# Kernel tuning notes

Measured on AMD Instinct MI355X. Metric: run time of the kernel, lower is better.

## Reference

```python
import jax, jax.numpy as jnp
import numpy as np

N_EMBED = 1024
EMBED_DIM = 64
BETA = 0.25


def setup_inputs() -> dict:
    key = jax.random.key(0)
    k1, k2 = jax.random.split(key)
    # z_e: (B, C, H, W) with C == embed_dim
    z_e = jax.random.normal(k1, (16, EMBED_DIM, 64, 64), dtype=jnp.float32)
    # codebook init: uniform(-1/n_embed, 1/n_embed), matching nn.init.uniform_
    emb = jax.random.uniform(k2, (N_EMBED, EMBED_DIM), dtype=jnp.float32,
                             minval=-1.0 / N_EMBED, maxval=1.0 / N_EMBED)
    return {"z_e": z_e, "emb": emb}


def reference(z_e, emb):
    B, C, H, W = z_e.shape
    # (B,C,H,W) -> (B,H,W,C) -> (B*H*W, C)
    z_flat = jnp.transpose(z_e, (0, 2, 3, 1)).reshape(-1, C)
    # squared euclidean distances to every codebook entry: (N, n_embed)
    dist = (jnp.sum(z_flat * z_flat, axis=1, keepdims=True)
            - 2.0 * (z_flat @ emb.T)
            + jnp.sum(emb * emb, axis=1)[None, :])
    idx = jnp.argmin(dist, axis=1)  # (N,)
    # gather codebook vectors, back to (B, C, H, W)
    z_q = jnp.transpose(emb[idx].reshape(B, H, W, C), (0, 3, 1, 2))
    # straight-through estimator
    z_q_st = z_e + jax.lax.stop_gradient(z_q - z_e)
    codebook_loss = jnp.mean((jax.lax.stop_gradient(z_q) - z_e) ** 2)
    commit_loss = jnp.mean((z_q - jax.lax.stop_gradient(z_e)) ** 2)
    loss = codebook_loss + BETA * commit_loss
    return z_q_st, loss, idx.reshape(B, H, W)
```

## Files before the change

kernel.cpp:

```cpp
#include <hip/hip_runtime.h>

#define NROWS   65536
#define NEMB    1024
#define HWD     4096
#define CHW     262144
#define OUT_ZQ  4194304
#define BETA    0.25f
#define MARGIN  6e-3f
#define MAXC    32

typedef __attribute__((ext_vector_type(8))) short bf16x8;
typedef __attribute__((ext_vector_type(4))) float f32x4;

#define F4C(v,i) ((i)==0?(v).x:((i)==1?(v).y:((i)==2?(v).z:(v).w)))

__device__ __forceinline__ unsigned short bf16rn(float f) {
    unsigned int x = __float_as_uint(f);
    x += 0x7fffu + ((x >> 16) & 1);
    return (unsigned short)(x >> 16);
}
__device__ __forceinline__ float bf16tof(unsigned short h) {
    return __uint_as_float(((unsigned int)h) << 16);
}
__device__ __forceinline__ unsigned int ordf(float f) {
    unsigned int u = __float_as_uint(f);
    return (u & 0x80000000u) ? ~u : (u | 0x80000000u);
}
__device__ __forceinline__ float deordf(unsigned int m) {
    return __uint_as_float((m & 0x80000000u) ? (m ^ 0x80000000u) : ~m);
}

__device__ __forceinline__ float np_pairwise64(const float p[64]) {
#pragma clang fp contract(off)
    float r[8];
#pragma unroll
    for (int a = 0; a < 8; ++a) r[a] = p[a];
#pragma unroll
    for (int i = 8; i < 64; i += 8) {
#pragma unroll
        for (int a = 0; a < 8; ++a) r[a] = r[a] + p[i + a];
    }
    return ((r[0] + r[1]) + (r[2] + r[3])) + ((r[4] + r[5]) + (r[6] + r[7]));
}

__global__ void k_prep(const float* __restrict__ emb, bf16x8* __restrict__ ebt,
                       float* __restrict__ se) {
#pragma clang fp contract(off)
    int idx  = blockIdx.x * 256 + threadIdx.x;
    int tile = idx >> 7;
    int f    = (idx >> 6) & 1;
    int lane = idx & 63;
    int entry = tile * 16 + (lane & 15);
    int kb    = f * 32 + ((lane >> 4) << 3);
    bf16x8 v;
#pragma unroll
    for (int i = 0; i < 8; ++i)
        v[i] = (short)bf16rn(emb[(size_t)entry * 64 + kb + i]);
    ebt[idx] = v;

    if (blockIdx.x < 4) {
        int j = blockIdx.x * 256 + threadIdx.x;
        float p[64];
#pragma unroll
        for (int c = 0; c < 64; ++c) { float vv = emb[(size_t)j * 64 + c]; p[c] = vv * vv; }
        se[j] = np_pairwise64(p);
    }
}

__global__ __launch_bounds__(256, 2) void k_mfma(
        const float* __restrict__ ze, const float* __restrict__ emb,
        const bf16x8* __restrict__ ebt, const float* __restrict__ se,
        float* __restrict__ out, float* __restrict__ wsloss) {
#pragma clang fp contract(off)
    __shared__ float zt[4096];
    __shared__ unsigned short zb[4096];
    __shared__ float se_s[NEMB];
    __shared__ float sz_s[64];
    __shared__ unsigned int rowmin_u[64];
    __shared__ int cnt_s[64];
    __shared__ int cand_s[64 * MAXC];
    __shared__ unsigned long long best_s[64];
    __shared__ int bi_s[64];

    const int tid  = threadIdx.x;
    const int wid  = tid >> 6;
    const int lane = tid & 63;
    const int l15  = lane & 15;
    const int kg   = lane >> 4;
    const int row0 = blockIdx.x * 64;
    const int b    = row0 >> 12;
    const int hw0  = row0 & 4095;
    const float* __restrict__ zblk = ze + (size_t)b * CHW + hw0;

#pragma unroll
    for (int k = 0; k < 4; ++k) se_s[k * 256 + tid] = se[k * 256 + tid];
#pragma unroll
    for (int k = 0; k < 16; ++k) {
        int idx = k * 256 + tid;
        zt[idx] = zblk[(size_t)(idx >> 6) * HWD + (idx & 63)];
    }
    if (tid < 64) { rowmin_u[tid] = 0xFFFFFFFFu; cnt_s[tid] = 0; best_s[tid] = ~0ULL; }
    __syncthreads();

    if (tid < 64) {
        float p[64];
#pragma unroll
        for (int c = 0; c < 64; ++c) { float v = zt[c * 64 + tid]; p[c] = v * v; }
        sz_s[tid] = np_pairwise64(p);
    }

#pragma unroll
    for (int k4 = 0; k4 < 2; ++k4) {
        int cid = k4 * 256 + tid;
        int row = cid >> 3, kc = cid & 7;
        bf16x8 v;
#pragma unroll
        for (int i = 0; i < 8; ++i) {
            int k = kc * 8 + i;
            v[i] = (short)bf16rn(zt[k * 64 + row]);
        }
        *(bf16x8*)&zb[(row * 64 + kc * 8) ^ ((row & 7) << 3)] = v;
    }
    __syncthreads();

    const int arow  = wid * 16 + l15;
    const int abase = arow * 64 + kg * 8;
    const int aswz  = (arow & 7) << 3;
    const bf16x8 Ah0 = *(const bf16x8*)&zb[(abase +  0) ^ aswz];
    const bf16x8 Ah1 = *(const bf16x8*)&zb[(abase + 32) ^ aswz];

    float rmin[4] = {3.4028235e38f, 3.4028235e38f, 3.4028235e38f, 3.4028235e38f};
    const bf16x8* __restrict__ ebt_l = ebt + lane;
    const f32x4 zero4 = {0.0f, 0.0f, 0.0f, 0.0f};
    bf16x8 Ca, Cb, Na, Nb;

#define LOADB(T, Xa, Xb) do {                                               \
        const bf16x8* p_ = ebt_l + (T) * 128;                               \
        Xa = p_[0]; Xb = p_[64];                                            \
    } while (0)

#define PROCESS(T, Xa, Xb, PASS2) do {                                      \
        f32x4 acc_ = zero4;                                                 \
        acc_ = __builtin_amdgcn_mfma_f32_16x16x32_bf16(Ah0, Xa, acc_, 0,0,0);\
        acc_ = __builtin_amdgcn_mfma_f32_16x16x32_bf16(Ah1, Xb, acc_, 0,0,0);\
        const int j_ = (T) * 16 + l15;                                      \
        const float sej_ = se_s[j_];                                        \
        _Pragma("unroll")                                                   \
        for (int q = 0; q < 4; ++q) {                                       \
            float g_ = fmaf(-2.0f, F4C(acc_, q), sej_);                     \
            if (!(PASS2)) {                                                 \
                rmin[q] = fminf(rmin[q], g_);                               \
            } else if (g_ <= rmin[q]) {                                     \
                int row_ = wid * 16 + kg * 4 + q;                           \
                int k_ = atomicAdd(&cnt_s[row_], 1);                        \
                if (k_ < MAXC) cand_s[row_ * MAXC + k_] = j_;               \
            }                                                               \
        }                                                                   \
    } while (0)

    LOADB(0, Ca, Cb);
    for (int t = 0; t < 64; t += 2) {
        LOADB(t + 1, Na, Nb);
        PROCESS(t, Ca, Cb, false);
        LOADB((t + 2 > 63 ? 63 : t + 2), Ca, Cb);
        PROCESS(t + 1, Na, Nb, false);
    }
#pragma unroll
    for (int q = 0; q < 4; ++q)
        atomicMin(&rowmin_u[wid * 16 + kg * 4 + q], ordf(rmin[q]));
    __syncthreads();
#pragma unroll
    for (int q = 0; q < 4; ++q)
        rmin[q] = deordf(rowmin_u[wid * 16 + kg * 4 + q]) + MARGIN;

    LOADB(0, Ca, Cb);
    for (int t = 0; t < 64; t += 2) {
        LOADB(t + 1, Na, Nb);
        PROCESS(t, Ca, Cb, true);
        LOADB((t + 2 > 63 ? 63 : t + 2), Ca, Cb);
        PROCESS(t + 1, Na, Nb, true);
    }
    __syncthreads();

    for (int w = tid; w < 64 * MAXC; w += 256) {
        int r = w >> 5, ci = w & (MAXC - 1);
        int nc = cnt_s[r];
        if (ci < (nc < MAXC ? nc : MAXC)) {
            int j = cand_s[r * MAXC + ci];
            const float* __restrict__ e = emb + (size_t)j * 64;
            float dot = 0.0f;
#pragma unroll
            for (int c = 0; c < 64; ++c) dot = fmaf(e[c], zt[c * 64 + r], dot);
            float d = (sz_s[r] - 2.0f * dot) + se_s[j];
            atomicMin(&best_s[r],
                      ((unsigned long long)ordf(d) << 32) | (unsigned int)j);
        }
        if (nc > MAXC) {
            for (int j = ci; j < NEMB; j += MAXC) {
                const float* __restrict__ e = emb + (size_t)j * 64;
                float dot = 0.0f;
#pragma unroll
                for (int c = 0; c < 64; ++c) dot = fmaf(e[c], zt[c * 64 + r], dot);
                float d = (sz_s[r] - 2.0f * dot) + se_s[j];
                atomicMin(&best_s[r],
                          ((unsigned long long)ordf(d) << 32) | (unsigned int)j);
            }
        }
    }
    __syncthreads();

    if (tid < 64) {
        int j = (int)(best_s[tid] & 0xFFFFFFFFu);
        bi_s[tid] = j;
        out[(size_t)OUT_ZQ + 1 + row0 + tid] = (float)j;
    }
    __syncthreads();

    float part = 0.0f;
#pragma unroll
    for (int rep = 0; rep < 16; ++rep) {
        int i = rep * 256 + tid;
        int c = i >> 6, r = i & 63;
        int bj = bi_s[r];
        size_t zoff = (size_t)b * CHW + (size_t)c * HWD + hw0 + r;
        float ev = emb[(size_t)bj * 64 + c];
        float zv = ze[zoff];
        float qmz = ev - zv;
        out[zoff] = zv + qmz;
        part = part + qmz * qmz;
    }
    float* red_s = (float*)cand_s;
    red_s[tid] = part;
    __syncthreads();
#pragma unroll
    for (int s = 128; s >= 1; s >>= 1) {
        if (tid < s) red_s[tid] = red_s[tid] + red_s[tid + s];
        __syncthreads();
    }
    if (tid == 0) wsloss[blockIdx.x] = red_s[0];
#undef LOADB
#undef PROCESS
}

__global__ __launch_bounds__(256, 4) void k_main_v5(
        const float* __restrict__ ze, const float* __restrict__ emb,
        const float* __restrict__ se, float* __restrict__ out,
        float* __restrict__ wsloss) {
#pragma clang fp contract(off)
    __shared__ float zt[4096];
    __shared__ float es[4096];
    __shared__ float se_s[NEMB];
    __shared__ float sz_s[64];
    __shared__ int   bi_s[64];

    const int tid  = threadIdx.x;
    const int rg   = tid & 15;
    const int eg   = tid >> 4;
    const int row0 = blockIdx.x * 64;
    const int b    = row0 >> 12;
    const int hw0  = row0 & 4095;
    const float* __restrict__ zblk = ze + (size_t)b * CHW + hw0;

#pragma unroll
    for (int k = 0; k < 4; ++k) se_s[k * 256 + tid] = se[k * 256 + tid];
#pragma unroll
    for (int k = 0; k < 16; ++k) {
        int idx = k * 256 + tid;
        zt[idx] = zblk[(size_t)(idx >> 6) * HWD + (idx & 63)];
    }
    __syncthreads();
    if (tid < 64) {
        float p[64];
#pragma unroll
        for (int c = 0; c < 64; ++c) { float v = zt[c * 64 + tid]; p[c] = v * v; }
        sz_s[tid] = np_pairwise64(p);
    }
    __syncthreads();
    const float4 sz4 = *(const float4*)&sz_s[rg * 4];
    float best[4] = {3.4028235e38f, 3.4028235e38f, 3.4028235e38f, 3.4028235e38f};
    int   bi[4]   = {0, 0, 0, 0};
    for (int ch = 0; ch < 16; ++ch) {
        __syncthreads();
        {
            const float4* __restrict__ src = (const float4*)(emb + ch * 4096);
#pragma unroll
            for (int k = 0; k < 4; ++k) {
                int idx = k * 256 + tid;
                int jl = idx >> 4, c4 = idx & 15;
                *(float4*)&es[(jl << 6) + ((c4 ^ (jl & 15)) << 2)] = src[idx];
            }
        }
        __syncthreads();
        const float4 se4 = *(const float4*)&se_s[ch * 64 + eg * 4];
        float acc[4][4];
#pragma unroll
        for (int a = 0; a < 4; ++a)
#pragma unroll
            for (int q = 0; q < 4; ++q) acc[a][q] = 0.0f;
#pragma unroll 4
        for (int c4 = 0; c4 < 16; ++c4) {
            float4 zq[4], ef[4];
#pragma unroll
            for (int cc = 0; cc < 4; ++cc)
                zq[cc] = *(const float4*)&zt[((c4 * 4 + cc) << 6) + (rg << 2)];
#pragma unroll
            for (int jj = 0; jj < 4; ++jj) {
                int jl = eg * 4 + jj;
                ef[jj] = *(const float4*)&es[(jl << 6) + ((c4 ^ (jl & 15)) << 2)];
            }
#pragma unroll
            for (int cc = 0; cc < 4; ++cc)
#pragma unroll
                for (int jj = 0; jj < 4; ++jj)
#pragma unroll
                    for (int rr = 0; rr < 4; ++rr)
                        acc[jj][rr] = fmaf(F4C(ef[jj], cc), F4C(zq[cc], rr), acc[jj][rr]);
        }
        const int j0 = ch * 64 + eg * 4;
#pragma unroll
        for (int jj = 0; jj < 4; ++jj) {
            float sej = F4C(se4, jj);
#pragma unroll
            for (int rr = 0; rr < 4; ++rr) {
                float dist = (F4C(sz4, rr) - 2.0f * acc[jj][rr]) + sej;
                if (dist < best[rr]) { best[rr] = dist; bi[rr] = j0 + jj; }
            }
        }
    }
    __syncthreads();
    float* dmin_s = zt;
    int*   imin_s = (int*)es;
#pragma unroll
    for (int rr = 0; rr < 4; ++rr) {
        dmin_s[tid * 4 + rr] = best[rr];
        imin_s[tid * 4 + rr] = bi[rr];
    }
    __syncthreads();
    if (tid < 64) {
        int rgm = tid >> 2, rrm = tid & 3;
        float bb = 3.4028235e38f; int ii = 0x7fffffff;
#pragma unroll
        for (int m = 0; m < 16; ++m) {
            int t = m * 16 + rgm;
            float d  = dmin_s[t * 4 + rrm];
            int   i2 = imin_s[t * 4 + rrm];
            if (d < bb || (d == bb && i2 < ii)) { bb = d; ii = i2; }
        }
        bi_s[tid] = ii;
        out[(size_t)OUT_ZQ + 1 + row0 + tid] = (float)ii;
    }
    __syncthreads();
    float part = 0.0f;
#pragma unroll
    for (int rep = 0; rep < 16; ++rep) {
        int i = rep * 256 + tid;
        int c = i >> 6, r = i & 63;
        int bj = bi_s[r];
        size_t zoff = (size_t)b * CHW + (size_t)c * HWD + hw0 + r;
        float ev = emb[(size_t)bj * 64 + c];
        float zv = ze[zoff];
        float qmz = ev - zv;
        out[zoff] = zv + qmz;
        part = part + qmz * qmz;
    }
    float* red_s = zt;
    red_s[tid] = part;
    __syncthreads();
#pragma unroll
    for (int s = 128; s >= 1; s >>= 1) {
        if (tid < s) red_s[tid] = red_s[tid] + red_s[tid + s];
        __syncthreads();
    }
    if (tid == 0) wsloss[blockIdx.x] = red_s[0];
}

__global__ void k_loss(const float* __restrict__ wsloss, float* __restrict__ out) {
#pragma clang fp contract(off)
    __shared__ float red[256];
    int tid = threadIdx.x;
    float s = 0.0f;
    for (int i = tid; i < 1024; i += 256) s = s + wsloss[i];
    red[tid] = s;
    __syncthreads();
#pragma unroll
    for (int k = 128; k >= 1; k >>= 1) {
        if (tid < k) red[tid] = red[tid] + red[tid + k];
        __syncthreads();
    }
    if (tid == 0) {
        float mse = red[0] / 4194304.0f;
        out[OUT_ZQ] = mse + BETA * mse;
    }
}

extern "C" void kernel_launch(void* const* d_in, const int* in_sizes, int n_in,
                              void* d_out, int out_size, void* d_ws, size_t ws_size,
                              hipStream_t stream) {
    const float* ze  = (const float*)d_in[0];
    const float* emb = (const float*)d_in[1];
    float* out    = (float*)d_out;
    float* se     = (float*)d_ws;
    float* wsloss = se + NEMB;
    bf16x8* ebt   = (bf16x8*)(wsloss + 1024);
    const size_t NEED = 2048 * sizeof(float) + 8192 * sizeof(bf16x8);

    if (ws_size >= NEED) {
        k_prep<<<32,   256, 0, stream>>>(emb, ebt, se);
        k_mfma<<<1024, 256, 0, stream>>>(ze, emb, ebt, se, out, wsloss);
    } else {
        k_prep<<<32, 256, 0, stream>>>(emb, (bf16x8*)d_ws, se);
        k_main_v5<<<1024, 256, 0, stream>>>(ze, emb, se, out, wsloss);
    }
    k_loss<<<1, 256, 0, stream>>>(wsloss, out);
}
```

Measured before the change: 130.4 us.

## Use split-bf16 A operand in MFMA screening, halve rows per block

The z operand becomes a hi+lo bf16 pair, so each 16x16 tile now takes four MFMAs instead of two. This gives more accurate screening distances, which lets the margin shrink and the per-row candidate cap drop from 32 to 16. Each block now handles 32 rows, with the four waves split as two row halves by two codebook halves, and the grid doubles to 2048 blocks. The aim is fewer fp32 rescoring candidates, less LDS per block and more blocks in flight, at the cost of twice the MFMA work and a higher chance of the fallback path when more than 16 candidates survive.

Result: slower. 173.4 us (+33.0%).

```diff
diff --git a/kernel.cpp b/kernel.cpp
--- a/kernel.cpp
+++ b/kernel.cpp
@@ -6,8 +6,8 @@
 #define CHW     262144
 #define OUT_ZQ  4194304
 #define BETA    0.25f
-#define MARGIN  6e-3f
-#define MAXC    32
+#define MARGIN  4e-3f
+#define MAXC    16
 
 typedef __attribute__((ext_vector_type(8))) short bf16x8;
 typedef __attribute__((ext_vector_type(4))) float f32x4;
@@ -72,22 +72,24 @@
         const bf16x8* __restrict__ ebt, const float* __restrict__ se,
         float* __restrict__ out, float* __restrict__ wsloss) {
 #pragma clang fp contract(off)
-    __shared__ float zt[4096];
+    __shared__ float zt[2048];
     __shared__ unsigned short zb[4096];
     __shared__ float se_s[NEMB];
-    __shared__ float sz_s[64];
-    __shared__ unsigned int rowmin_u[64];
-    __shared__ int cnt_s[64];
-    __shared__ int cand_s[64 * MAXC];
-    __shared__ unsigned long long best_s[64];
-    __shared__ int bi_s[64];
+    __shared__ float sz_s[32];
+    __shared__ unsigned int rowmin_u[32];
+    __shared__ int cnt_s[32];
+    __shared__ int cand_s[32 * MAXC];
+    __shared__ unsigned long long best_s[32];
+    __shared__ int bi_s[32];
 
     const int tid  = threadIdx.x;
     const int wid  = tid >> 6;
     const int lane = tid & 63;
     const int l15  = lane & 15;
     const int kg   = lane >> 4;
-    const int row0 = blockIdx.x * 64;
+    const int rh   = wid >> 1;
+    const int eh   = wid & 1;
+    const int row0 = blockIdx.x * 32;
     const int b    = row0 >> 12;
     const int hw0  = row0 & 4095;
     const float* __restrict__ zblk = ze + (size_t)b * CHW + hw0;
@@ -95,42 +97,46 @@
 #pragma unroll
     for (int k = 0; k < 4; ++k) se_s[k * 256 + tid] = se[k * 256 + tid];
 #pragma unroll
-    for (int k = 0; k < 16; ++k) {
+    for (int k = 0; k < 8; ++k) {
         int idx = k * 256 + tid;
-        zt[idx] = zblk[(size_t)(idx >> 6) * HWD + (idx & 63)];
-    }
-    if (tid < 64) { rowmin_u[tid] = 0xFFFFFFFFu; cnt_s[tid] = 0; best_s[tid] = ~0ULL; }
-    __syncthreads();
-
-    if (tid < 64) {
+        zt[idx] = zblk[(size_t)(idx >> 5) * HWD + (idx & 31)];
+    }
+    if (tid < 32) { rowmin_u[tid] = 0xFFFFFFFFu; cnt_s[tid] = 0; best_s[tid] = ~0ULL; }
+    __syncthreads();
+
+    if (tid < 32) {
         float p[64];
 #pragma unroll
-        for (int c = 0; c < 64; ++c) { float v = zt[c * 64 + tid]; p[c] = v * v; }
+        for (int c = 0; c < 64; ++c) { float v = zt[c * 32 + tid]; p[c] = v * v; }
         sz_s[tid] = np_pairwise64(p);
     }
 
 #pragma unroll
     for (int k4 = 0; k4 < 2; ++k4) {
         int cid = k4 * 256 + tid;
-        int row = cid >> 3, kc = cid & 7;
+        int row = cid >> 4, kc = cid & 15;
         bf16x8 v;
 #pragma unroll
         for (int i = 0; i < 8; ++i) {
             int k = kc * 8 + i;
-            v[i] = (short)bf16rn(zt[k * 64 + row]);
-        }
-        *(bf16x8*)&zb[(row * 64 + kc * 8) ^ ((row & 7) << 3)] = v;
-    }
-    __syncthreads();
-
-    const int arow  = wid * 16 + l15;
-    const int abase = arow * 64 + kg * 8;
+            float z = zt[(k & 63) * 32 + row];
+            unsigned short h = bf16rn(z);
+            v[i] = (short)((k < 64) ? h : bf16rn(z - bf16tof(h)));
+        }
+        *(bf16x8*)&zb[(row * 128 + kc * 8) ^ ((row & 7) << 3)] = v;
+    }
+    __syncthreads();
+
+    const int arow  = rh * 16 + l15;
+    const int abase = arow * 128 + kg * 8;
     const int aswz  = (arow & 7) << 3;
     const bf16x8 Ah0 = *(const bf16x8*)&zb[(abase +  0) ^ aswz];
     const bf16x8 Ah1 = *(const bf16x8*)&zb[(abase + 32) ^ aswz];
+    const bf16x8 Al0 = *(const bf16x8*)&zb[(abase + 64) ^ aswz];
+    const bf16x8 Al1 = *(const bf16x8*)&zb[(abase + 96) ^ aswz];
 
     float rmin[4] = {3.4028235e38f, 3.4028235e38f, 3.4028235e38f, 3.4028235e38f};
-    const bf16x8* __restrict__ ebt_l = ebt + lane;
+    const bf16x8* __restrict__ ebt_l = ebt + (size_t)eh * 32 * 128 + lane;
     const f32x4 zero4 = {0.0f, 0.0f, 0.0f, 0.0f};
     bf16x8 Ca, Cb, Na, Nb;
 
@@ -143,7 +149,9 @@
         f32x4 acc_ = zero4;                                                 \
         acc_ = __builtin_amdgcn_mfma_f32_16x16x32_bf16(Ah0, Xa, acc_, 0,0,0);\
         acc_ = __builtin_amdgcn_mfma_f32_16x16x32_bf16(Ah1, Xb, acc_, 0,0,0);\
-        const int j_ = (T) * 16 + l15;                                      \
+        acc_ = __builtin_amdgcn_mfma_f32_16x16x32_bf16(Al0, Xa, acc_, 0,0,0);\
+        acc_ = __builtin_amdgcn_mfma_f32_16x16x32_bf16(Al1, Xb, acc_, 0,0,0);\
+        const int j_ = (eh * 32 + (T)) * 16 + l15;                          \
         const float sej_ = se_s[j_];                                        \
         _Pragma("unroll")                                                   \
         for (int q = 0; q < 4; ++q) {                                       \
@@ -151,7 +159,7 @@
             if (!(PASS2)) {                                                 \
                 rmin[q] = fminf(rmin[q], g_);                               \
             } else if (g_ <= rmin[q]) {                                     \
-                int row_ = wid * 16 + kg * 4 + q;                           \
+                int row_ = rh * 16 + kg * 4 + q;                            \
                 int k_ = atomicAdd(&cnt_s[row_], 1);                        \
                 if (k_ < MAXC) cand_s[row_ * MAXC + k_] = j_;               \
             }                                                               \
@@ -159,38 +167,38 @@
     } while (0)
 
     LOADB(0, Ca, Cb);
-    for (int t = 0; t < 64; t += 2) {
+    for (int t = 0; t < 32; t += 2) {
         LOADB(t + 1, Na, Nb);
         PROCESS(t, Ca, Cb, false);
-        LOADB((t + 2 > 63 ? 63 : t + 2), Ca, Cb);
+        LOADB((t + 2 > 31 ? 31 : t + 2), Ca, Cb);
         PROCESS(t + 1, Na, Nb, false);
     }
 #pragma unroll
     for (int q = 0; q < 4; ++q)
-        atomicMin(&rowmin_u[wid * 16 + kg * 4 + q], ordf(rmin[q]));
+        atomicMin(&rowmin_u[rh * 16 + kg * 4 + q], ordf(rmin[q]));
     __syncthreads();
 #pragma unroll
     for (int q = 0; q < 4; ++q)
-        rmin[q] = deordf(rowmin_u[wid * 16 + kg * 4 + q]) + MARGIN;
+        rmin[q] = deordf(rowmin_u[rh * 16 + kg * 4 + q]) + MARGIN;
 
     LOADB(0, Ca, Cb);
-    for (int t = 0; t < 64; t += 2) {
+    for (int t = 0; t < 32; t += 2) {
         LOADB(t + 1, Na, Nb);
         PROCESS(t, Ca, Cb, true);
-        LOADB((t + 2 > 63 ? 63 : t + 2), Ca, Cb);
+        LOADB((t + 2 > 31 ? 31 : t + 2), Ca, Cb);
         PROCESS(t + 1, Na, Nb, true);
     }
     __syncthreads();
 
-    for (int w = tid; w < 64 * MAXC; w += 256) {
-        int r = w >> 5, ci = w & (MAXC - 1);
+    for (int w = tid; w < 32 * MAXC; w += 256) {
+        int r = w >> 4, ci = w & (MAXC - 1);
         int nc = cnt_s[r];
         if (ci < (nc < MAXC ? nc : MAXC)) {
             int j = cand_s[r * MAXC + ci];
             const float* __restrict__ e = emb + (size_t)j * 64;
             float dot = 0.0f;
 #pragma unroll
-            for (int c = 0; c < 64; ++c) dot = fmaf(e[c], zt[c * 64 + r], dot);
+            for (int c = 0; c < 64; ++c) dot = fmaf(e[c], zt[c * 32 + r], dot);
             float d = (sz_s[r] - 2.0f * dot) + se_s[j];
             atomicMin(&best_s[r],
                       ((unsigned long long)ordf(d) << 32) | (unsigned int)j);
@@ -200,7 +208,7 @@
                 const float* __restrict__ e = emb + (size_t)j * 64;
                 float dot = 0.0f;
 #pragma unroll
-                for (int c = 0; c < 64; ++c) dot = fmaf(e[c], zt[c * 64 + r], dot);
+                for (int c = 0; c < 64; ++c) dot = fmaf(e[c], zt[c * 32 + r], dot);
                 float d = (sz_s[r] - 2.0f * dot) + se_s[j];
                 atomicMin(&best_s[r],
                           ((unsigned long long)ordf(d) << 32) | (unsigned int)j);
@@ -209,13 +217,147 @@
     }
     __syncthreads();
 
-    if (tid < 64) {
+    if (tid < 32) {
         int j = (int)(best_s[tid] & 0xFFFFFFFFu);
         bi_s[tid] = j;
         out[(size_t)OUT_ZQ + 1 + row0 + tid] = (float)j;
     }
     __syncthreads();
 
+    float part = 0.0f;
+#pragma unroll
+    for (int rep = 0; rep < 8; ++rep) {
+        int i = rep * 256 + tid;
+        int c = i >> 5, r = i & 31;
+        int bj = bi_s[r];
+        size_t zoff = (size_t)b * CHW + (size_t)c * HWD + hw0 + r;
+        float ev = emb[(size_t)bj * 64 + c];
+        float zv = ze[zoff];
+        float qmz = ev - zv;
+        out[zoff] = zv + qmz;
+        part = part + qmz * qmz;
+    }
+    float* red_s = (float*)zb;
+    red_s[tid] = part;
+    __syncthreads();
+#pragma unroll
+    for (int s = 128; s >= 1; s >>= 1) {
+        if (tid < s) red_s[tid] = red_s[tid] + red_s[tid + s];
+        __syncthreads();
+    }
+    if (tid == 0) wsloss[blockIdx.x] = red_s[0];
+#undef LOADB
+#undef PROCESS
+}
+
+__global__ __launch_bounds__(256, 4) void k_main_v5(
+        const float* __restrict__ ze, const float* __restrict__ emb,
+        const float* __restrict__ se, float* __restrict__ out,
+        float* __restrict__ wsloss) {
+#pragma clang fp contract(off)
+    __shared__ float zt[4096];
+    __shared__ float es[4096];
+    __shared__ float se_s[NEMB];
+    __shared__ float sz_s[64];
+    __shared__ int   bi_s[64];
+
+    const int tid  = threadIdx.x;
+    const int rg   = tid & 15;
+    const int eg   = tid >> 4;
+    const int row0 = blockIdx.x * 64;
+    const int b    = row0 >> 12;
+    const int hw0  = row0 & 4095;
+    const float* __restrict__ zblk = ze + (size_t)b * CHW + hw0;
+
+#pragma unroll
+    for (int k = 0; k < 4; ++k) se_s[k * 256 + tid] = se[k * 256 + tid];
+#pragma unroll
+    for (int k = 0; k < 16; ++k) {
+        int idx = k * 256 + tid;
+        zt[idx] = zblk[(size_t)(idx >> 6) * HWD + (idx & 63)];
+    }
+    __syncthreads();
+    if (tid < 64) {
+        float p[64];
+#pragma unroll
+        for (int c = 0; c < 64; ++c) { float v = zt[c * 64 + tid]; p[c] = v * v; }
+        sz_s[tid] = np_pairwise64(p);
+    }
+    __syncthreads();
+    const float4 sz4 = *(const float4*)&sz_s[rg * 4];
+    float best[4] = {3.4028235e38f, 3.4028235e38f, 3.4028235e38f, 3.4028235e38f};
+    int   bi[4]   = {0, 0, 0, 0};
+    for (int ch = 0; ch < 16; ++ch) {
+        __syncthreads();
+        {
+            const float4* __restrict__ src = (const float4*)(emb + ch * 4096);
+#pragma unroll
+            for (int k = 0; k < 4; ++k) {
+                int idx = k * 256 + tid;
+                int jl = idx >> 4, c4 = idx & 15;
+                *(float4*)&es[(jl << 6) + ((c4 ^ (jl & 15)) << 2)] = src[idx];
+            }
+        }
+        __syncthreads();
+        const float4 se4 = *(const float4*)&se_s[ch * 64 + eg * 4];
+        float acc[4][4];
+#pragma unroll
+        for (int a = 0; a < 4; ++a)
+#pragma unroll
+            for (int q = 0; q < 4; ++q) acc[a][q] = 0.0f;
+#pragma unroll 4
+        for (int c4 = 0; c4 < 16; ++c4) {
+            float4 zq[4], ef[4];
+#pragma unroll
+            for (int cc = 0; cc < 4; ++cc)
+                zq[cc] = *(const float4*)&zt[((c4 * 4 + cc) << 6) + (rg << 2)];
+#pragma unroll
+            for (int jj = 0; jj < 4; ++jj) {
+                int jl = eg * 4 + jj;
+                ef[jj] = *(const float4*)&es[(jl << 6) + ((c4 ^ (jl & 15)) << 2)];
+            }
+#pragma unroll
+            for (int cc = 0; cc < 4; ++cc)
+#pragma unroll
+                for (int jj = 0; jj < 4; ++jj)
+#pragma unroll
+                    for (int rr = 0; rr < 4; ++rr)
+                        acc[jj][rr] = fmaf(F4C(ef[jj], cc), F4C(zq[cc], rr), acc[jj][rr]);
+        }
+        const int j0 = ch * 64 + eg * 4;
+#pragma unroll
+        for (int jj = 0; jj < 4; ++jj) {
+            float sej = F4C(se4, jj);
+#pragma unroll
+            for (int rr = 0; rr < 4; ++rr) {
+                float dist = (F4C(sz4, rr) - 2.0f * acc[jj][rr]) + sej;
+                if (dist < best[rr]) { best[rr] = dist; bi[rr] = j0 + jj; }
+            }
+        }
+    }
+    __syncthreads();
+    float* dmin_s = zt;
+    int*   imin_s = (int*)es;
+#pragma unroll
+    for (int rr = 0; rr < 4; ++rr) {
+        dmin_s[tid * 4 + rr] = best[rr];
+        imin_s[tid * 4 + rr] = bi[rr];
+    }
+    __syncthreads();
+    if (tid < 64) {
+        int rgm = tid >> 2, rrm = tid & 3;
+        float bb = 3.4028235e38f; int ii = 0x7fffffff;
+#pragma unroll
+        for (int m = 0; m < 16; ++m) {
+            int t = m * 16 + rgm;
+            float d  = dmin_s[t * 4 + rrm];
+            int   i2 = imin_s[t * 4 + rrm];
+            if (d < bb || (d == bb && i2 < ii)) { bb = d; ii = i2; }
+        }
+        bi_s[tid] = ii;
+        out[(size_t)OUT_ZQ + 1 + row0 + tid] = (float)ii;
+    }
+    __syncthreads();
     float part = 0.0f;
 #pragma unroll
     for (int rep = 0; rep < 16; ++rep) {
@@ -229,7 +371,7 @@
         out[zoff] = zv + qmz;
         part = part + qmz * qmz;
     }
-    float* red_s = (float*)cand_s;
+    float* red_s = zt;
     red_s[tid] = part;
     __syncthreads();
 #pragma unroll
@@ -238,148 +380,15 @@
         __syncthreads();
     }
     if (tid == 0) wsloss[blockIdx.x] = red_s[0];
-#undef LOADB
-#undef PROCESS
-}
-
-__global__ __launch_bounds__(256, 4) void k_main_v5(
-        const float* __restrict__ ze, const float* __restrict__ emb,
-        const float* __restrict__ se, float* __restrict__ out,
-        float* __restrict__ wsloss) {
-#pragma clang fp contract(off)
-    __shared__ float zt[4096];
-    __shared__ float es[4096];
-    __shared__ float se_s[NEMB];
-    __shared__ float sz_s[64];
-    __shared__ int   bi_s[64];
-
-    const int tid  = threadIdx.x;
-    const int rg   = tid & 15;
-    const int eg   = tid >> 4;
-    const int row0 = blockIdx.x * 64;
-    const int b    = row0 >> 12;
-    const int hw0  = row0 & 4095;
-    const float* __restrict__ zblk = ze + (size_t)b * CHW + hw0;
-
-#pragma unroll
-    for (int k = 0; k < 4; ++k) se_s[k * 256 + tid] = se[k * 256 + tid];
-#pragma unroll
-    for (int k = 0; k < 16; ++k) {
-        int idx = k * 256 + tid;
-        zt[idx] = zblk[(size_t)(idx >> 6) * HWD + (idx & 63)];
-    }
-    __syncthreads();
-    if (tid < 64) {
-        float p[64];
-#pragma unroll
-        for (int c = 0; c < 64; ++c) { float v = zt[c * 64 + tid]; p[c] = v * v; }
-        sz_s[tid] = np_pairwise64(p);
-    }
-    __syncthreads();
-    const float4 sz4 = *(const float4*)&sz_s[rg * 4];
-    float best[4] = {3.4028235e38f, 3.4028235e38f, 3.4028235e38f, 3.4028235e38f};
-    int   bi[4]   = {0, 0, 0, 0};
-    for (int ch = 0; ch < 16; ++ch) {
-        __syncthreads();
-        {
-            const float4* __restrict__ src = (const float4*)(emb + ch * 4096);
-#pragma unroll
-            for (int k = 0; k < 4; ++k) {
-                int idx = k * 256 + tid;
-                int jl = idx >> 4, c4 = idx & 15;
-                *(float4*)&es[(jl << 6) + ((c4 ^ (jl & 15)) << 2)] = src[idx];
-            }
-        }
-        __syncthreads();
-        const float4 se4 = *(const float4*)&se_s[ch * 64 + eg * 4];
-        float acc[4][4];
-#pragma unroll
-        for (int a = 0; a < 4; ++a)
-#pragma unroll
-            for (int q = 0; q < 4; ++q) acc[a][q] = 0.0f;
-#pragma unroll 4
-        for (int c4 = 0; c4 < 16; ++c4) {
-            float4 zq[4], ef[4];
-#pragma unroll
-            for (int cc = 0; cc < 4; ++cc)
-                zq[cc] = *(const float4*)&zt[((c4 * 4 + cc) << 6) + (rg << 2)];
-#pragma unroll
-            for (int jj = 0; jj < 4; ++jj) {
-                int jl = eg * 4 + jj;
-                ef[jj] = *(const float4*)&es[(jl << 6) + ((c4 ^ (jl & 15)) << 2)];
-            }
-#pragma unroll
-            for (int cc = 0; cc < 4; ++cc)
-#pragma unroll
-                for (int jj = 0; jj < 4; ++jj)
-#pragma unroll
-                    for (int rr = 0; rr < 4; ++rr)
-                        acc[jj][rr] = fmaf(F4C(ef[jj], cc), F4C(zq[cc], rr), acc[jj][rr]);
-        }
-        const int j0 = ch * 64 + eg * 4;
-#pragma unroll
-        for (int jj = 0; jj < 4; ++jj) {
-            float sej = F4C(se4, jj);
-#pragma unroll
-            for (int rr = 0; rr < 4; ++rr) {
-                float dist = (F4C(sz4, rr) - 2.0f * acc[jj][rr]) + sej;
-                if (dist < best[rr]) { best[rr] = dist; bi[rr] = j0 + jj; }
-            }
-        }
-    }
-    __syncthreads();
-    float* dmin_s = zt;
-    int*   imin_s = (int*)es;
-#pragma unroll
-    for (int rr = 0; rr < 4; ++rr) {
-        dmin_s[tid * 4 + rr] = best[rr];
-        imin_s[tid * 4 + rr] = bi[rr];
-    }
-    __syncthreads();
-    if (tid < 64) {
-        int rgm = tid >> 2, rrm = tid & 3;
-        float bb = 3.4028235e38f; int ii = 0x7fffffff;
-#pragma unroll
-        for (int m = 0; m < 16; ++m) {
-            int t = m * 16 + rgm;
-            float d  = dmin_s[t * 4 + rrm];
-            int   i2 = imin_s[t * 4 + rrm];
-            if (d < bb || (d == bb && i2 < ii)) { bb = d; ii = i2; }
-        }
-        bi_s[tid] = ii;
-        out[(size_t)OUT_ZQ + 1 + row0 + tid] = (float)ii;
-    }
-    __syncthreads();
-    float part = 0.0f;
-#pragma unroll
-    for (int rep = 0; rep < 16; ++rep) {
-        int i = rep * 256 + tid;
-        int c = i >> 6, r = i & 63;
-        int bj = bi_s[r];
-        size_t zoff = (size_t)b * CHW + (size_t)c * HWD + hw0 + r;
-        float ev = emb[(size_t)bj * 64 + c];
-        float zv = ze[zoff];
-        float qmz = ev - zv;
-        out[zoff] = zv + qmz;
-        part = part + qmz * qmz;
-    }
-    float* red_s = zt;
-    red_s[tid] = part;
-    __syncthreads();
-#pragma unroll
-    for (int s = 128; s >= 1; s >>= 1) {
-        if (tid < s) red_s[tid] = red_s[tid] + red_s[tid + s];
-        __syncthreads();
-    }
-    if (tid == 0) wsloss[blockIdx.x] = red_s[0];
-}
-
-__global__ void k_loss(const float* __restrict__ wsloss, float* __restrict__ out) {
+}
+
+__global__ void k_loss(const float* __restrict__ wsloss, float* __restrict__ out,
+                       int nblk) {
 #pragma clang fp contract(off)
     __shared__ float red[256];
     int tid = threadIdx.x;
     float s = 0.0f;
-    for (int i = tid; i < 1024; i += 256) s = s + wsloss[i];
+    for (int i = tid; i < nblk; i += 256) s = s + wsloss[i];
     red[tid] = s;
     __syncthreads();
 #pragma unroll
@@ -401,15 +410,16 @@
     float* out    = (float*)d_out;
     float* se     = (float*)d_ws;
     float* wsloss = se + NEMB;
-    bf16x8* ebt   = (bf16x8*)(wsloss + 1024);
-    const size_t NEED = 2048 * sizeof(float) + 8192 * sizeof(bf16x8);
+    bf16x8* ebt   = (bf16x8*)(wsloss + 2048);
+    const size_t NEED = (1024 + 2048) * sizeof(float) + 8192 * sizeof(bf16x8);
 
     if (ws_size >= NEED) {
         k_prep<<<32,   256, 0, stream>>>(emb, ebt, se);
-        k_mfma<<<1024, 256, 0, stream>>>(ze, emb, ebt, se, out, wsloss);
+        k_mfma<<<2048, 256, 0, stream>>>(ze, emb, ebt, se, out, wsloss);
+        k_loss<<<1, 256, 0, stream>>>(wsloss, out, 2048);
     } else {
         k_prep<<<32, 256, 0, stream>>>(emb, (bf16x8*)d_ws, se);
         k_main_v5<<<1024, 256, 0, stream>>>(ze, emb, se, out, wsloss);
-    }
-    k_loss<<<1, 256, 0, stream>>>(wsloss, out);
-}
+        k_loss<<<1, 256, 0, stream>>>(wsloss, out, 1024);
+    }
+}
```
